# Performance work log

Hardware: AMD Instinct MI355X
Metric: run time of the kernel (lower is better)

The kernel has to match this reference:

```python
import jax, jax.numpy as jnp
import numpy as np


def setup_inputs() -> dict:
    key = jax.random.key(0)
    k0, k1, k2, k3 = jax.random.split(key, 4)
    B, M, H, K, OUT = 256, 64, 64, 128, 256
    x0 = jax.random.normal(k0, (B, M, K), dtype=jnp.float32)
    xl = jax.random.normal(k1, (B, H, K), dtype=jnp.float32)
    # Conv1d(in_channels=M*H, out_channels=OUT, kernel_size=1) params
    fan_in = M * H  # kernel_size=1
    bound = 1.0 / np.sqrt(fan_in)
    W = jax.random.uniform(k2, (OUT, M * H, 1), dtype=jnp.float32, minval=-bound, maxval=bound)
    b = jax.random.uniform(k3, (OUT,), dtype=jnp.float32, minval=-bound, maxval=bound)
    return {"x0": x0, "xl": xl, "k": K, "W": W, "b": b}


def reference(x0, xl, k, W, b):
    # x0: [B, m, k_emb], xl: [B, h, k_emb]
    # Fused equivalent of the per-column loop: for each embedding column i,
    # matmul(xl[:,:,i:i+1], x0[:,:,i:i+1]^T) -> [B,h,m]; stacked over k -> [B,h,m,k]
    fmap = jnp.einsum('bhk,bmk->bhmk', xl, x0)
    B = x0.shape[0]
    h, m = xl.shape[1], x0.shape[1]
    fmap = fmap.reshape(B, h * m, k)  # [B, h*m, k]
    # 1x1 Conv1d == GEMM over channel dim
    out = jnp.einsum('bck,oc->bok', fmap, W[:, :, 0]) + b[None, :, None]
    return out
```

## Files before the change

kernel.cpp:

```cpp
#include <hip/hip_runtime.h>
#include <hip/hip_bf16.h>
#include <stdint.h>


typedef __attribute__((ext_vector_type(8)))  short short8;
typedef __attribute__((ext_vector_type(16))) float f32x16;

#define B_SZ   256
#define K_SZ   128
#define OUT_SZ 256
#define C_SZ   4096
#define NH     64

__device__ __forceinline__ uint32_t pack_bf16(float a, float b) {
    __hip_bfloat162 h2 = __float22bfloat162_rn(make_float2(a, b));
    union { __hip_bfloat162 h; uint32_t u; } v;
    v.h = h2;
    return v.u;
}

__device__ __forceinline__ float bf2f(short s) {
    union { uint32_t u; float f; } v;
    v.u = ((uint32_t)(uint16_t)s) << 16;
    return v.f;
}

__device__ __forceinline__ void load_lds_16(const void* g, void* l) {
    __builtin_amdgcn_global_load_lds(
        (const __attribute__((address_space(1))) unsigned int*)g,
        (__attribute__((address_space(3))) unsigned int*)l,
        16, 0, 0);
}

__global__ void convert_W_tiled(const float* __restrict__ W, short* __restrict__ Wb) {
    int t = blockIdx.x * blockDim.x + threadIdx.x;
    int lane = t & 63;
    int sub  = t >> 6;
    int cb16 = sub & 255;
    int got  = sub >> 8;
    int o = got * 32 + (lane & 31);
    int c = cb16 * 16 + (lane >> 5) * 8;
    const float* p = W + (size_t)o * C_SZ + c;
    float4 w0 = *(const float4*)p;
    float4 w1 = *(const float4*)(p + 4);
    union { short8 s; uint32_t u[4]; } cc;
    cc.u[0] = pack_bf16(w0.x, w0.y);
    cc.u[1] = pack_bf16(w0.z, w0.w);
    cc.u[2] = pack_bf16(w1.x, w1.y);
    cc.u[3] = pack_bf16(w1.z, w1.w);
    *(short8*)(Wb + (size_t)t * 8) = cc.s;
}

template<bool USE_WS>
__global__ __launch_bounds__(512, 2)
void cin_main(const float* __restrict__ x0, const float* __restrict__ xl,
              const float* __restrict__ Wf, const short* __restrict__ Wb,
              const float* __restrict__ bias, float* __restrict__ out) {
    __shared__ short Wlds[4 * 16384];
    __shared__ short xls[NH * K_SZ];

    const int b    = blockIdx.x;
    const int tid  = threadIdx.x;
    const int lane = tid & 63;
    const int wave = tid >> 6;
    const int l31  = lane & 31;
    const int hi   = lane >> 5;

    {
        const float4* src = (const float4*)(xl + (size_t)b * (NH * K_SZ));
        float4 v[4];
#pragma unroll
        for (int i = 0; i < 4; ++i) v[i] = src[tid * 4 + i];
        uint32_t* dst = (uint32_t*)&xls[tid * 16];
#pragma unroll
        for (int i = 0; i < 4; ++i) {
            dst[2 * i]     = pack_bf16(v[i].x, v[i].y);
            dst[2 * i + 1] = pack_bf16(v[i].z, v[i].w);
        }
    }

    union { short8 s; uint32_t u[4]; } x0p[4][4];
    {
        const float* x0b = x0 + (size_t)b * (64 * K_SZ);
#pragma unroll
        for (int s = 0; s < 4; ++s)
#pragma unroll
            for (int nt = 0; nt < 4; ++nt)
#pragma unroll
                for (int t2 = 0; t2 < 4; ++t2) {
                    const int m0 = s * 16 + hi * 8 + 2 * t2;
                    const int cc = nt * 32 + l31;
                    x0p[s][nt].u[t2] = pack_bf16(x0b[m0 * K_SZ + cc],
                                                 x0b[(m0 + 1) * K_SZ + cc]);
                }
    }

    const short* wsrc = Wb + ((size_t)wave * 256) * 512 + lane * 8;
    const float* wfrow = Wf + (size_t)(wave * 32 + l31) * C_SZ + hi * 8;

    auto stage = [&](int buf, int h) {
        short* d = Wlds + buf * 16384 + wave * 2048;
        if (USE_WS) {
            const short* s0 = wsrc + (size_t)(4 * h) * 512;
#pragma unroll
            for (int cbl = 0; cbl < 4; ++cbl)
                load_lds_16(s0 + cbl * 512, d + cbl * 512);
        } else {
#pragma unroll
            for (int cbl = 0; cbl < 4; ++cbl) {
                const float* p = wfrow + h * 64 + cbl * 16;
                float4 w0 = *(const float4*)p;
                float4 w1 = *(const float4*)(p + 4);
                union { short8 s; uint32_t u[4]; } cc;
                cc.u[0] = pack_bf16(w0.x, w0.y);
                cc.u[1] = pack_bf16(w0.z, w0.w);
                cc.u[2] = pack_bf16(w1.x, w1.y);
                cc.u[3] = pack_bf16(w1.z, w1.w);
                *(short8*)(d + cbl * 512 + lane * 8) = cc.s;
            }
        }
    };

    f32x16 acc[4];
#pragma unroll
    for (int nt = 0; nt < 4; ++nt)
#pragma unroll
        for (int r = 0; r < 16; ++r) acc[nt][r] = 0.f;
    f32x16 kz;
#pragma unroll
    for (int r = 0; r < 16; ++r) kz[r] = 0.f;

    __syncthreads();
    stage(0, 0);
    stage(1, 1);
    stage(2, 2);

    for (int h = 0; h < NH; ++h) {
        if (!USE_WS) asm volatile("s_waitcnt lgkmcnt(0)" ::: "memory");
        asm volatile("s_waitcnt vmcnt(8)" ::: "memory");
        __builtin_amdgcn_s_barrier();

        stage((h + 3) & 3, (h + 3) & (NH - 1));

        const short* wb2 = Wlds + (h & 3) * 16384 + wave * 2048 + lane * 8;
        const short8 af0 = *(const short8*)(wb2);
        const short8 af1 = *(const short8*)(wb2 + 512);
        const short8 af2 = *(const short8*)(wb2 + 1024);
        const short8 af3 = *(const short8*)(wb2 + 1536);

        float xlv[4];
#pragma unroll
        for (int nt = 0; nt < 4; ++nt)
            xlv[nt] = bf2f(xls[h * K_SZ + nt * 32 + l31]);

        __builtin_amdgcn_s_setprio(1);
#pragma unroll
        for (int nt = 0; nt < 4; ++nt) {
            f32x16 g = __builtin_amdgcn_mfma_f32_32x32x16_bf16(af0, x0p[0][nt].s, kz, 0, 0, 0);
            g = __builtin_amdgcn_mfma_f32_32x32x16_bf16(af1, x0p[1][nt].s, g, 0, 0, 0);
            g = __builtin_amdgcn_mfma_f32_32x32x16_bf16(af2, x0p[2][nt].s, g, 0, 0, 0);
            g = __builtin_amdgcn_mfma_f32_32x32x16_bf16(af3, x0p[3][nt].s, g, 0, 0, 0);
#pragma unroll
            for (int r = 0; r < 16; ++r)
                acc[nt][r] += xlv[nt] * g[r];
        }
        __builtin_amdgcn_s_setprio(0);
    }

    float bv[16];
#pragma unroll
    for (int r = 0; r < 16; ++r)
        bv[r] = bias[wave * 32 + (r & 3) + 8 * (r >> 2) + 4 * hi];

    float* outb = out + (size_t)b * (OUT_SZ * K_SZ);
#pragma unroll
    for (int nt = 0; nt < 4; ++nt) {
        const int kcol = nt * 32 + l31;
#pragma unroll
        for (int r = 0; r < 16; ++r) {
            const int orow = wave * 32 + (r & 3) + 8 * (r >> 2) + 4 * hi;
            outb[orow * K_SZ + kcol] = acc[nt][r] + bv[r];
        }
    }
}

extern "C" void kernel_launch(void* const* d_in, const int* in_sizes, int n_in,
                              void* d_out, int out_size, void* d_ws, size_t ws_size,
                              hipStream_t stream) {
    const float* x0   = (const float*)d_in[0];
    const float* xl   = (const float*)d_in[1];
    const float* W    = (const float*)d_in[3];
    const float* bias = (const float*)d_in[4];
    float* out = (float*)d_out;

    const size_t w_bytes = (size_t)OUT_SZ * C_SZ * sizeof(short);
    short* Wb = (short*)d_ws;

    if (ws_size >= w_bytes) {
        convert_W_tiled<<<dim3(512), dim3(256), 0, stream>>>(W, Wb);
        cin_main<true><<<dim3(B_SZ), dim3(512), 0, stream>>>(x0, xl, W, Wb, bias, out);
    } else {
        cin_main<false><<<dim3(B_SZ), dim3(512), 0, stream>>>(x0, xl, W, Wb, bias, out);
    }
}
```

Measured before the change: 92.33 us.

## Split output channels across two blocks per batch and use per-wave W pipeline

Launches two 256-thread blocks per batch element, each covering half the output channels, which doubles the grid to 512 blocks. Each wave now stages only its own W slice into a private 3-deep LDS ring with global_load_lds, so the per-iteration block barrier and setprio are removed. This cuts LDS use and should raise occupancy and overlap. The cost is that each x0 tile is loaded and converted twice, and there is no barrier protecting the ring buffer reuse across waves, though each wave only touches its own slice.

```diff
diff --git a/kernel.cpp b/kernel.cpp
--- a/kernel.cpp
+++ b/kernel.cpp
@@ -52,30 +52,30 @@
 }
 
 template<bool USE_WS>
-__global__ __launch_bounds__(512, 2)
+__global__ __launch_bounds__(256, 2)
 void cin_main(const float* __restrict__ x0, const float* __restrict__ xl,
               const float* __restrict__ Wf, const short* __restrict__ Wb,
               const float* __restrict__ bias, float* __restrict__ out) {
-    __shared__ short Wlds[4 * 16384];
+    __shared__ short Wlds[4 * 3 * 2048];
     __shared__ short xls[NH * K_SZ];
 
-    const int b    = blockIdx.x;
-    const int tid  = threadIdx.x;
-    const int lane = tid & 63;
-    const int wave = tid >> 6;
-    const int l31  = lane & 31;
-    const int hi   = lane >> 5;
+    const int b     = blockIdx.y;
+    const int ohalf = blockIdx.x;
+    const int tid   = threadIdx.x;
+    const int lane  = tid & 63;
+    const int wave  = tid >> 6;
+    const int got   = ohalf * 4 + wave;
+    const int l31   = lane & 31;
+    const int hi    = lane >> 5;
 
     {
         const float4* src = (const float4*)(xl + (size_t)b * (NH * K_SZ));
-        float4 v[4];
-#pragma unroll
-        for (int i = 0; i < 4; ++i) v[i] = src[tid * 4 + i];
-        uint32_t* dst = (uint32_t*)&xls[tid * 16];
-#pragma unroll
-        for (int i = 0; i < 4; ++i) {
-            dst[2 * i]     = pack_bf16(v[i].x, v[i].y);
-            dst[2 * i + 1] = pack_bf16(v[i].z, v[i].w);
+        uint32_t* dst = (uint32_t*)&xls[tid * 32];
+#pragma unroll
+        for (int i = 0; i < 8; ++i) {
+            float4 v = src[tid * 8 + i];
+            dst[2 * i]     = pack_bf16(v.x, v.y);
+            dst[2 * i + 1] = pack_bf16(v.z, v.w);
         }
     }
 
@@ -95,20 +95,21 @@
                 }
     }
 
-    const short* wsrc = Wb + ((size_t)wave * 256) * 512 + lane * 8;
-    const float* wfrow = Wf + (size_t)(wave * 32 + l31) * C_SZ + hi * 8;
+    const short* wsrc  = Wb + ((size_t)got * 256) * 512 + lane * 8;
+    const float* wfrow = Wf + (size_t)(got * 32 + l31) * C_SZ + hi * 8;
+    short* wl = Wlds + wave * (3 * 2048);
 
     auto stage = [&](int buf, int h) {
-        short* d = Wlds + buf * 16384 + wave * 2048;
         if (USE_WS) {
             const short* s0 = wsrc + (size_t)(4 * h) * 512;
-#pragma unroll
-            for (int cbl = 0; cbl < 4; ++cbl)
-                load_lds_16(s0 + cbl * 512, d + cbl * 512);
+            short* d = wl + buf * 2048;
+#pragma unroll
+            for (int sub = 0; sub < 4; ++sub)
+                load_lds_16(s0 + sub * 512, d + sub * 512);
         } else {
 #pragma unroll
-            for (int cbl = 0; cbl < 4; ++cbl) {
-                const float* p = wfrow + h * 64 + cbl * 16;
+            for (int sub = 0; sub < 4; ++sub) {
+                const float* p = wfrow + h * 64 + sub * 16;
                 float4 w0 = *(const float4*)p;
                 float4 w1 = *(const float4*)(p + 4);
                 union { short8 s; uint32_t u[4]; } cc;
@@ -116,7 +117,7 @@
                 cc.u[1] = pack_bf16(w0.z, w0.w);
                 cc.u[2] = pack_bf16(w1.x, w1.y);
                 cc.u[3] = pack_bf16(w1.z, w1.w);
-                *(short8*)(d + cbl * 512 + lane * 8) = cc.s;
+                *(short8*)(wl + buf * 2048 + sub * 512 + lane * 8) = cc.s;
             }
         }
     };
@@ -130,19 +131,18 @@
 #pragma unroll
     for (int r = 0; r < 16; ++r) kz[r] = 0.f;
 
-    __syncthreads();
     stage(0, 0);
     stage(1, 1);
-    stage(2, 2);
-
+    __syncthreads();
+
+    int buf = 0;
     for (int h = 0; h < NH; ++h) {
-        if (!USE_WS) asm volatile("s_waitcnt lgkmcnt(0)" ::: "memory");
-        asm volatile("s_waitcnt vmcnt(8)" ::: "memory");
-        __builtin_amdgcn_s_barrier();
-
-        stage((h + 3) & 3, (h + 3) & (NH - 1));
-
-        const short* wb2 = Wlds + (h & 3) * 16384 + wave * 2048 + lane * 8;
+        if (USE_WS) asm volatile("s_waitcnt vmcnt(4)" ::: "memory");
+
+        int bn = buf + 2; if (bn >= 3) bn -= 3;
+        stage(bn, (h + 2) & (NH - 1));
+
+        const short* wb2 = wl + buf * 2048 + lane * 8;
         const short8 af0 = *(const short8*)(wb2);
         const short8 af1 = *(const short8*)(wb2 + 512);
         const short8 af2 = *(const short8*)(wb2 + 1024);
@@ -153,7 +153,6 @@
         for (int nt = 0; nt < 4; ++nt)
             xlv[nt] = bf2f(xls[h * K_SZ + nt * 32 + l31]);
 
-        __builtin_amdgcn_s_setprio(1);
 #pragma unroll
         for (int nt = 0; nt < 4; ++nt) {
             f32x16 g = __builtin_amdgcn_mfma_f32_32x32x16_bf16(af0, x0p[0][nt].s, kz, 0, 0, 0);
@@ -164,13 +163,14 @@
             for (int r = 0; r < 16; ++r)
                 acc[nt][r] += xlv[nt] * g[r];
         }
-        __builtin_amdgcn_s_setprio(0);
+
+        buf += 1; if (buf == 3) buf = 0;
     }
 
     float bv[16];
 #pragma unroll
     for (int r = 0; r < 16; ++r)
-        bv[r] = bias[wave * 32 + (r & 3) + 8 * (r >> 2) + 4 * hi];
+        bv[r] = bias[got * 32 + (r & 3) + 8 * (r >> 2) + 4 * hi];
 
     float* outb = out + (size_t)b * (OUT_SZ * K_SZ);
 #pragma unroll
@@ -178,7 +178,7 @@
         const int kcol = nt * 32 + l31;
 #pragma unroll
         for (int r = 0; r < 16; ++r) {
-            const int orow = wave * 32 + (r & 3) + 8 * (r >> 2) + 4 * hi;
+            const int orow = got * 32 + (r & 3) + 8 * (r >> 2) + 4 * hi;
             outb[orow * K_SZ + kcol] = acc[nt][r] + bv[r];
         }
     }
@@ -198,8 +198,8 @@
 
     if (ws_size >= w_bytes) {
         convert_W_tiled<<<dim3(512), dim3(256), 0, stream>>>(W, Wb);
-        cin_main<true><<<dim3(B_SZ), dim3(512), 0, stream>>>(x0, xl, W, Wb, bias, out);
+        cin_main<true><<<dim3(2, B_SZ), dim3(256), 0, stream>>>(x0, xl, W, Wb, bias, out);
     } else {
-        cin_main<false><<<dim3(B_SZ), dim3(512), 0, stream>>>(x0, xl, W, Wb, bias, out);
-    }
-}
+        cin_main<false><<<dim3(2, B_SZ), dim3(256), 0, stream>>>(x0, xl, W, Wb, bias, out);
+    }
+}
```

Result: faster. 79.16 us (-14.3%).
